# Performance work log

Hardware: AMD Instinct MI355X
Metric: run time of the kernel (lower is better)

Reference implementation:

```python
import jax, jax.numpy as jnp
import numpy as np

N_HEAD = 16

def rel_shift(x):
    # x: (qlen, klen, B, n). Pad one zero column at front of klen axis,
    # reinterpret as (klen+1, qlen, B, n), drop first row, reshape back.
    qlen, klen, b, n = x.shape
    x_pad = jnp.pad(x, ((0, 0), (1, 0), (0, 0), (0, 0)))
    x_pad = x_pad.reshape(klen + 1, qlen, b, n)
    return x_pad[1:].reshape(qlen, klen, b, n)

def setup_inputs() -> dict:
    key = jax.random.key(0)
    ks = jax.random.split(key, 9)
    qlen = klen = 1024
    B = 4
    d_model = 1024
    d_head = d_model // N_HEAD
    q = jax.random.normal(ks[0], (qlen, B, d_model), jnp.float32)
    K = jax.random.normal(ks[1], (klen, B, d_model), jnp.float32)
    V = jax.random.normal(ks[2], (klen, B, d_model), jnp.float32)
    mask = jax.random.bernoulli(ks[3], 0.1, (1, klen, B, 1))
    r = jax.random.normal(ks[4], (klen, d_model), jnp.float32)
    u = jax.random.normal(ks[5], (N_HEAD, d_head), jnp.float32) * 0.02
    v = jax.random.normal(ks[6], (N_HEAD, d_head), jnp.float32) * 0.02
    Wr = jax.random.normal(ks[7], (d_model, d_model), jnp.float32) / np.sqrt(d_model)
    br = jax.random.normal(ks[8], (d_model,), jnp.float32) * 0.02
    return {"q": q, "K": K, "V": V, "mask": mask, "r": r, "u": u, "v": v, "Wr": Wr, "br": br}

def reference(q, K, V, mask, r, u, v, Wr, br):
    qlen, bsz, d_model = q.shape
    klen = K.shape[0]
    d_head = d_model // N_HEAD
    qh = q.reshape(qlen, bsz, N_HEAD, d_head)
    Kh = K.reshape(klen, bsz, N_HEAD, d_head)
    Vh = V.reshape(klen, bsz, N_HEAD, d_head)
    rh = (r @ Wr.T + br).reshape(klen, N_HEAD, d_head)  # r_net projection
    AC = jnp.einsum('ibnd,jbnd->ijbn', qh + u, Kh)
    BD = rel_shift(jnp.einsum('ibnd,jnd->ijbn', qh + v, rh))
    score = (AC + BD) / jnp.sqrt(jnp.asarray(d_head, q.dtype))
    # mask (1,klen,B,1) broadcasts over qlen and heads (torch repeats over heads)
    score = jnp.where(mask, jnp.asarray(-1e9, score.dtype), score)
    weight = jax.nn.softmax(score, axis=1)
    out = jnp.einsum('ijbn,jbnd->ibnd', weight, Vh).reshape(qlen, bsz, d_model)
    return out, weight.mean(axis=-1)
```

## Files before the change

kernel.cpp:

```cpp
#include <hip/hip_runtime.h>
#include <hip/hip_fp16.h>
#include <stdint.h>


#define L 1024
#define BATCH 4
#define NH 16
#define DH 64
#define DM 1024
#define TI 16
#define NJT 16
#define BDP_ST 1032
#define SCALE 0.125f
#define CS 0.18033688011112042f

typedef __attribute__((ext_vector_type(8))) short short8;
typedef __attribute__((ext_vector_type(4))) float f32x4;

static __device__ __forceinline__ unsigned short f2bf(float f) {
    union { float f; unsigned int u; } x; x.f = f;
    return (unsigned short)((x.u + 0x7fffu + ((x.u >> 16) & 1u)) >> 16);
}
static __device__ __forceinline__ float bf2f(unsigned short h) {
    union { unsigned int u; float f; } x; x.u = ((unsigned int)h) << 16;
    return x.f;
}
static __device__ __forceinline__ unsigned short f2h(float f) {
    __half h = __float2half(f);
    union { __half h; unsigned short s; } x; x.h = h; return x.s;
}
static __device__ __forceinline__ float h2f(unsigned short s) {
    union { __half h; unsigned short s; } x; x.s = s; return __half2float(x.h);
}
static __device__ __forceinline__ unsigned short* usp(void* base, int byteoff) {
    return (unsigned short*)((char*)base + byteoff);
}
static __device__ __forceinline__ short8 ld8(const void* base, int byteoff) {
    return *(const short8*)((const char*)base + byteoff);
}
static __device__ __forceinline__ float fexp2(float x) {
#if __has_builtin(__builtin_amdgcn_exp2f)
    return __builtin_amdgcn_exp2f(x);
#else
    return __expf(x * 0.6931471805599453f);
#endif
}
#define SW128(row, colByte) ((((row) * 128) + (colByte)) ^ (((row) & 7) << 4))

__global__ __launch_bounds__(256) void rh_gemm_mfma(
    const float* __restrict__ r, const float* __restrict__ Wr,
    const float* __restrict__ br, unsigned short* __restrict__ rhb)
{
    __shared__ unsigned short rT[64 * 64];
    __shared__ unsigned short wT[64 * 64];
    const int c0 = blockIdx.x * 64, m0 = blockIdx.y * 64;
    const int tid = threadIdx.x;
    const int w = tid >> 6, lane = tid & 63, lr = lane & 15, lg = lane >> 4;
    f32x4 acc[4] = {};

    for (int kt = 0; kt < 16; ++kt) {
        const int k0 = kt * 64;
        __syncthreads();
        const int row = tid >> 2, cb = (tid & 3) * 16;
#pragma unroll
        for (int q4 = 0; q4 < 4; ++q4) {
            float4 rv = *(const float4*)(r + (size_t)(c0 + row) * DM + k0 + cb + q4 * 4);
            unsigned short* p = usp(rT, SW128(row, (cb + q4 * 4) * 2));
            p[0] = f2bf(rv.x); p[1] = f2bf(rv.y); p[2] = f2bf(rv.z); p[3] = f2bf(rv.w);
            float4 wv = *(const float4*)(Wr + (size_t)(m0 + row) * DM + k0 + cb + q4 * 4);
            unsigned short* pw = usp(wT, SW128(row, (cb + q4 * 4) * 2));
            pw[0] = f2bf(wv.x); pw[1] = f2bf(wv.y); pw[2] = f2bf(wv.z); pw[3] = f2bf(wv.w);
        }
        __syncthreads();
#pragma unroll
        for (int mch = 0; mch < 4; ++mch)
#pragma unroll
            for (int kh = 0; kh < 2; ++kh) {
                short8 a  = ld8(rT, SW128(w * 16 + lr,   (kh * 32 + lg * 8) * 2));
                short8 bb = ld8(wT, SW128(mch * 16 + lr, (kh * 32 + lg * 8) * 2));
                acc[mch] = __builtin_amdgcn_mfma_f32_16x16x32_bf16(a, bb, acc[mch], 0, 0, 0);
            }
    }
#pragma unroll
    for (int mch = 0; mch < 4; ++mch)
#pragma unroll
        for (int r2 = 0; r2 < 4; ++r2) {
            const int c = c0 + w * 16 + lg * 4 + r2;
            const int d = mch * 16 + lr;
            const float val = acc[mch][r2] + br[m0 + d];
            rhb[((size_t)blockIdx.y * L + c) * DH + d] = f2bf(val);
        }
}

__global__ __launch_bounds__(256) void rh_gemm_kernel(
    const float* __restrict__ r, const float* __restrict__ Wr,
    const float* __restrict__ br, float* __restrict__ rhf)
{
    __shared__ float As[16][65];
    __shared__ float Bs[16][65];
    const int j0 = blockIdx.x * 64;
    const int m0 = blockIdx.y * 64;
    const int tid = threadIdx.x;
    const int ty = tid >> 4, tx = tid & 15;
    float acc[4][4] = {};

    for (int k0 = 0; k0 < DM; k0 += 16) {
        const int row = tid >> 2, c4 = (tid & 3) << 2;
        float4 av = *(const float4*)(r  + (size_t)(j0 + row) * DM + k0 + c4);
        float4 bv = *(const float4*)(Wr + (size_t)(m0 + row) * DM + k0 + c4);
        __syncthreads();
        As[c4 + 0][row] = av.x; As[c4 + 1][row] = av.y;
        As[c4 + 2][row] = av.z; As[c4 + 3][row] = av.w;
        Bs[c4 + 0][row] = bv.x; Bs[c4 + 1][row] = bv.y;
        Bs[c4 + 2][row] = bv.z; Bs[c4 + 3][row] = bv.w;
        __syncthreads();
#pragma unroll
        for (int k = 0; k < 16; ++k) {
            float a[4], bb[4];
#pragma unroll
            for (int t = 0; t < 4; ++t) { a[t] = As[k][ty * 4 + t]; bb[t] = Bs[k][tx * 4 + t]; }
#pragma unroll
            for (int ii = 0; ii < 4; ++ii)
#pragma unroll
                for (int jj = 0; jj < 4; ++jj)
                    acc[ii][jj] = fmaf(a[ii], bb[jj], acc[ii][jj]);
        }
    }
#pragma unroll
    for (int ii = 0; ii < 4; ++ii) {
        const int row = j0 + ty * 4 + ii;
#pragma unroll
        for (int jj = 0; jj < 4; ++jj) {
            const int col = m0 + tx * 4 + jj;
            rhf[(size_t)row * DM + col] = acc[ii][jj] + br[col];
        }
    }
}

__global__ __launch_bounds__(256) void prepass_kernel(
    const float* __restrict__ Kg, const float* __restrict__ Vg,
    unsigned short* __restrict__ Kbf, unsigned short* __restrict__ Vtb)
{
    __shared__ unsigned short tile[64][80];
    const int j0 = blockIdx.x * 64;
    const int b = blockIdx.y, n = blockIdx.z;
    const int bn = b * NH + n;
    const int tid = threadIdx.x;

    for (int idx = tid; idx < 64 * 16; idx += 256) {
        const int jr = idx >> 4, s4 = (idx & 15) * 4;
        const size_t src = ((size_t)(j0 + jr) * BATCH + b) * DM + n * DH + s4;
        float4 kv = *(const float4*)(Kg + src);
        ushort4 o;
        o.x = f2bf(kv.x); o.y = f2bf(kv.y); o.z = f2bf(kv.z); o.w = f2bf(kv.w);
        *(ushort4*)(Kbf + ((size_t)bn * L + j0 + jr) * DH + s4) = o;
        float4 vv4 = *(const float4*)(Vg + src);
        tile[s4 + 0][jr] = f2bf(vv4.x); tile[s4 + 1][jr] = f2bf(vv4.y);
        tile[s4 + 2][jr] = f2bf(vv4.z); tile[s4 + 3][jr] = f2bf(vv4.w);
    }
    __syncthreads();
    for (int idx = tid; idx < 64 * 8; idx += 256) {
        const int d = idx >> 3, p8 = (idx & 7) * 8;
        short8 o = *(const short8*)&tile[d][p8];
        *(short8*)(Vtb + ((size_t)bn * DH + d) * L + j0 + p8) = o;
    }
}

__global__ __launch_bounds__(256) void wm_reduce_kernel(
    const unsigned short* __restrict__ Wf, const float* __restrict__ rdeng,
    float* __restrict__ wm_out)
{
    const int ig = blockIdx.x;
    const int b  = blockIdx.y;
    const int ib = ig >> 2, lg = ig & 3;
    const int tid = threadIdx.x;
#pragma unroll
    for (int jj = 0; jj < 4; ++jj) {
        const int j = jj * 256 + tid;
        const int gc = j >> 4, lr = j & 15;
        float a0 = 0.f, a1 = 0.f, a2 = 0.f, a3 = 0.f;
#pragma unroll
        for (int n = 0; n < NH; ++n) {
            const int bn = b * NH + n;
            const float4 rd = *(const float4*)(rdeng + ((size_t)bn << 10) + ig * 4);
            ushort4 wv = *(const ushort4*)(Wf +
                ((((size_t)bn * 64 + ib) * 64 + gc) * 64 + lg * 16 + lr) * 4);
            a0 += bf2f(wv.x) * rd.x; a1 += bf2f(wv.y) * rd.y;
            a2 += bf2f(wv.z) * rd.z; a3 += bf2f(wv.w) * rd.w;
        }
        const size_t o = ((size_t)(ig * 4) * L + j) * BATCH + b;
        wm_out[o]                      = a0;
        wm_out[o + (size_t)L * BATCH]  = a1;
        wm_out[o + 2 * (size_t)L * BATCH] = a2;
        wm_out[o + 3 * (size_t)L * BATCH] = a3;
    }
}

__global__ __launch_bounds__(256, 3) void attn_fused(
    const float* __restrict__ q,
    const unsigned short* __restrict__ Kbf, const unsigned short* __restrict__ Vtb,
    const unsigned char* __restrict__ maskp,
    const float* __restrict__ uu, const float* __restrict__ vvp,
    const unsigned short* __restrict__ rhb,
    float* __restrict__ out, unsigned short* __restrict__ W_ws,
    float* __restrict__ rdeng)
{
    __shared__ __align__(16) unsigned short BDp[17 * BDP_ST];
    __shared__ __align__(16) unsigned short Wt[4][2][16 * 64];
    __shared__ unsigned char mblk[L];
    __shared__ float denomP[4][16];
    __shared__ float rdenom[16];
    __shared__ int mflags;

    const int lin = blockIdx.x;
    const int xcd = lin & 7, idx = lin >> 3;
    const int ib  = idx & 63;
    const int pane = xcd * 8 + (idx >> 6);
    const int b = pane >> 4, n = pane & 15;
    const int i0 = ib * 16;
    const int bn = pane;

    const int tid = threadIdx.x;
    const int w = tid >> 6, lane = tid & 63, lr = lane & 15, lg = lane >> 4;

    if (tid == 0) mflags = 0;
    __syncthreads();
    {
        int local = 0;
        for (int ww = tid; ww < 1024; ww += 256) {
            const unsigned int word = ((const unsigned int*)maskp)[ww];
            if (word == 0x3f800000u) local |= 1;
            else if (word & 0xffffff00u) local |= 2;
        }
        if (local) atomicOr(&mflags, local);
    }
    __syncthreads();
    {
        const int mtype = (mflags & 1) ? 2 : ((mflags & 2) ? 1 : 0);
        for (int j = tid; j < L; j += 256) {
            bool mv;
            if (mtype == 2)      mv = ((const float*)maskp)[j * BATCH + b] != 0.f;
            else if (mtype == 1) mv = maskp[j * BATCH + b] != 0;
            else                 mv = ((const int*)maskp)[j * BATCH + b] != 0;
            mblk[j] = mv ? 1 : 0;
        }
    }
    if (tid < 17 * 8) {
        const int row = tid >> 3, cp = tid & 7;
        BDp[row * BDP_ST + 1024 + cp] = 0;
    }

    const float* qrow = q + ((size_t)(i0 + lr) * BATCH + b) * DM + n * DH;
    const float* urow = uu + n * DH;
    const float* vrow = vvp + n * DH;
    short8 qu_a[2], qv_a[2];
#pragma unroll
    for (int kh = 0; kh < 2; ++kh) {
        const int kb = kh * 32 + lg * 8;
        float4 qa = *(const float4*)(qrow + kb), qb = *(const float4*)(qrow + kb + 4);
        float4 ua = *(const float4*)(urow + kb), ub = *(const float4*)(urow + kb + 4);
        float4 va = *(const float4*)(vrow + kb), vb = *(const float4*)(vrow + kb + 4);
        short8 su, sv;
        su[0] = (short)f2bf((qa.x + ua.x) * CS); su[1] = (short)f2bf((qa.y + ua.y) * CS);
        su[2] = (short)f2bf((qa.z + ua.z) * CS); su[3] = (short)f2bf((qa.w + ua.w) * CS);
        su[4] = (short)f2bf((qb.x + ub.x) * CS); su[5] = (short)f2bf((qb.y + ub.y) * CS);
        su[6] = (short)f2bf((qb.z + ub.z) * CS); su[7] = (short)f2bf((qb.w + ub.w) * CS);
        sv[0] = (short)f2bf((qa.x + va.x) * CS); sv[1] = (short)f2bf((qa.y + va.y) * CS);
        sv[2] = (short)f2bf((qa.z + va.z) * CS); sv[3] = (short)f2bf((qa.w + va.w) * CS);
        sv[4] = (short)f2bf((qb.x + vb.x) * CS); sv[5] = (short)f2bf((qb.y + vb.y) * CS);
        sv[6] = (short)f2bf((qb.z + vb.z) * CS); sv[7] = (short)f2bf((qb.w + vb.w) * CS);
        qu_a[kh] = su; qv_a[kh] = sv;
    }
    float qv16[16];
    {
        const int kq = (tid & 3) * 16;
        if (i0 + 16 < L) {
            const float* q16 = q + ((size_t)(i0 + 16) * BATCH + b) * DM + n * DH;
#pragma unroll
            for (int e4 = 0; e4 < 4; ++e4) {
                float4 qa = *(const float4*)(q16 + kq + e4 * 4);
                float4 va = *(const float4*)(vrow + kq + e4 * 4);
                qv16[e4 * 4 + 0] = (qa.x + va.x) * CS; qv16[e4 * 4 + 1] = (qa.y + va.y) * CS;
                qv16[e4 * 4 + 2] = (qa.z + va.z) * CS; qv16[e4 * 4 + 3] = (qa.w + va.w) * CS;
            }
        } else {
#pragma unroll
            for (int e = 0; e < 16; ++e) qv16[e] = 0.f;
        }
    }

    {
        const unsigned short* rpane = rhb + (size_t)n * L * DH;
        const int ccol = w * 16 + lr;
        short8 rb[2][2];
#pragma unroll
        for (int kh = 0; kh < 2; ++kh) {
            rb[0][kh] = *(const short8*)(rpane + (size_t)ccol * DH + kh * 32 + lg * 8);
            rb[1][kh] = *(const short8*)(rpane + (size_t)(64 + ccol) * DH + kh * 32 + lg * 8);
        }
        const int col16 = tid >> 2;
        const int kq = (tid & 3) * 16;
#pragma unroll
        for (int ct = 0; ct < 16; ++ct) {
            const int c0 = ct * 64;
            const int cur = ct & 1;
            short8 nk0, nk1;
            if (ct + 2 < 16) {
                nk0 = *(const short8*)(rpane + (size_t)((ct + 2) * 64 + ccol) * DH + lg * 8);
                nk1 = *(const short8*)(rpane + (size_t)((ct + 2) * 64 + ccol) * DH + 32 + lg * 8);
            }
            f32x4 acc = {0.f, 0.f, 0.f, 0.f};
#pragma unroll
            for (int kh = 0; kh < 2; ++kh)
                acc = __builtin_amdgcn_mfma_f32_16x16x32_bf16(qv_a[kh], rb[cur][kh], acc, 0, 0, 0);
#pragma unroll
            for (int r2 = 0; r2 < 4; ++r2)
                BDp[(lg * 4 + r2) * BDP_ST + c0 + ccol] = f2h(acc[r2]);
            {
                short8 ra0 = *(const short8*)(rpane + (size_t)(c0 + col16) * DH + kq);
                short8 ra1 = *(const short8*)(rpane + (size_t)(c0 + col16) * DH + kq + 8);
                float s16 = 0.f;
#pragma unroll
                for (int e = 0; e < 8; ++e) {
                    s16 = fmaf(qv16[e],     bf2f((unsigned short)ra0[e]), s16);
                    s16 = fmaf(qv16[e + 8], bf2f((unsigned short)ra1[e]), s16);
                }
                s16 += __shfl_xor(s16, 1);
                s16 += __shfl_xor(s16, 2);
                if ((tid & 3) == 0) BDp[16 * BDP_ST + c0 + col16] = f2h(s16);
            }
            if (ct + 2 < 16) { rb[cur][0] = nk0; rb[cur][1] = nk1; }
        }
    }
    __syncthreads();

    const unsigned short* Kpane = Kbf + (size_t)bn * L * DH;
    const unsigned short* Vpane = Vtb + (size_t)bn * DH * L;
    const int jwbase = w * 256;
    f32x4 pv[4] = {};
    float dl[4] = {0.f, 0.f, 0.f, 0.f};
    int ilb[4];
#pragma unroll
    for (int r2 = 0; r2 < 4; ++r2) ilb[r2] = (lg * 4 + r2) * BDP_ST;

    short8 kf[2][2];
#pragma unroll
    for (int kh = 0; kh < 2; ++kh) {
        kf[0][kh] = *(const short8*)(Kpane + (size_t)(jwbase + lr) * DH + kh * 32 + lg * 8);
        kf[1][kh] = *(const short8*)(Kpane + (size_t)(jwbase + 16 + lr) * DH + kh * 32 + lg * 8);
    }

#pragma unroll 1
    for (int sub = 0; sub < 4; ++sub) {
        const int jbase = jwbase + sub * 64;
        unsigned short* WtW = &Wt[w][sub & 1][0];
        short8 vfr[8];
#pragma unroll
        for (int dch = 0; dch < 4; ++dch)
#pragma unroll
            for (int kh = 0; kh < 2; ++kh)
                vfr[dch * 2 + kh] = *(const short8*)(Vpane + (size_t)(dch * 16 + lr) * L + jbase + kh * 32 + lg * 8);
#pragma unroll
        for (int c4 = 0; c4 < 4; ++c4) {
            const int chunk = sub * 4 + c4;
            const int cur = c4 & 1;
            short8 nk0, nk1;
            if (chunk + 2 < 16) {
                const int jn = jwbase + (chunk + 2) * 16 + lr;
                nk0 = *(const short8*)(Kpane + (size_t)jn * DH + lg * 8);
                nk1 = *(const short8*)(Kpane + (size_t)jn * DH + 32 + lg * 8);
            }
            f32x4 acc = {0.f, 0.f, 0.f, 0.f};
#pragma unroll
            for (int kh = 0; kh < 2; ++kh)
                acc = __builtin_amdgcn_mfma_f32_16x16x32_bf16(qu_a[kh], kf[cur][kh], acc, 0, 0, 0);
            const int gj = jbase + c4 * 16 + lr;
            const float mo = mblk[gj] ? -1e9f : 0.f;
            const int ebase = gj - i0 - lg * 4;
            ushort4 wpack;
#pragma unroll
            for (int r2 = 0; r2 < 4; ++r2) {
                const int e = ebase - r2;
                const int addr = ilb[r2] + e + ((e <= 0) ? 1023 : 1030);
                const float bd = h2f(BDp[addr]);
                float s = fminf(acc[r2] + bd + mo, 126.f);
                const float wg = fexp2(s);
                dl[r2] += wg;
                const unsigned short wb = f2bf(wg);
                ((unsigned short*)&wpack)[r2] = wb;
                *usp(WtW, SW128(lg * 4 + r2, (c4 * 16 + lr) * 2)) = wb;
            }
            {
                const int gc = w * 16 + chunk - w * 16 + jwbase / 16 + 0;
                const int gcc = (jbase >> 4) + c4;
                *(ushort4*)(W_ws + ((((size_t)bn * 64 + ib) * 64 + gcc) * 64 + lane) * 4) = wpack;
                (void)gc;
            }
            if (chunk + 2 < 16) { kf[cur][0] = nk0; kf[cur][1] = nk1; }
        }
#pragma unroll
        for (int dch = 0; dch < 4; ++dch)
#pragma unroll
            for (int kh = 0; kh < 2; ++kh) {
                short8 a = ld8(WtW, SW128(lr, (kh * 32 + lg * 8) * 2));
                pv[dch] = __builtin_amdgcn_mfma_f32_16x16x32_bf16(a, vfr[dch * 2 + kh], pv[dch], 0, 0, 0);
            }
    }

#pragma unroll
    for (int r2 = 0; r2 < 4; ++r2) {
        float d = dl[r2];
        d += __shfl_xor(d, 1); d += __shfl_xor(d, 2);
        d += __shfl_xor(d, 4); d += __shfl_xor(d, 8);
        if (lr == 0) denomP[w][lg * 4 + r2] = d;
    }
    {
        float* pvw = (float*)&Wt[w][0][0];
#pragma unroll
        for (int dch = 0; dch < 4; ++dch)
#pragma unroll
            for (int r2 = 0; r2 < 4; ++r2)
                pvw[(lg * 4 + r2) * 64 + dch * 16 + lr] = pv[dch][r2];
    }
    __syncthreads();
    if (tid < 16) {
        const float dn = denomP[0][tid] + denomP[1][tid] + denomP[2][tid] + denomP[3][tid];
        rdenom[tid] = 1.f / dn;
        rdeng[((size_t)bn << 10) + i0 + tid] = 1.f / (dn * 16.f);
    }
    __syncthreads();

    {
        const float* pvwAll = (const float*)&Wt[0][0][0];
        const int il = tid >> 4, d0 = (tid & 15) * 4;
        float4 o  = *(const float4*)(pvwAll + 0 * 1024 + il * 64 + d0);
        float4 o1 = *(const float4*)(pvwAll + 1 * 1024 + il * 64 + d0);
        float4 o2 = *(const float4*)(pvwAll + 2 * 1024 + il * 64 + d0);
        float4 o3 = *(const float4*)(pvwAll + 3 * 1024 + il * 64 + d0);
        const float rs = rdenom[il];
        o.x = (o.x + o1.x + o2.x + o3.x) * rs;
        o.y = (o.y + o1.y + o2.y + o3.y) * rs;
        o.z = (o.z + o1.z + o2.z + o3.z) * rs;
        o.w = (o.w + o1.w + o2.w + o3.w) * rs;
        *(float4*)(out + ((size_t)(i0 + il) * BATCH + b) * DM + n * DH + d0) = o;
    }
}

template<int MODE>
__global__ __launch_bounds__(256, 2) void attn_legacy(
    const float* __restrict__ q,
    const void* __restrict__ Kp, const void* __restrict__ Vp,
    const unsigned char* __restrict__ maskp,
    const float* __restrict__ uu, const float* __restrict__ vvp,
    const void* __restrict__ rhp,
    float* __restrict__ out, float* __restrict__ wm_out)
{
    __shared__ unsigned short QU[16 * 64];
    __shared__ unsigned short QV[17 * 64];
    __shared__ unsigned short KR[(MODE == 1) ? 64 * 64 : 8];
    __shared__ unsigned short VT[(MODE == 1) ? 64 * 64 : 8];
    __shared__ unsigned short BDp[17 * BDP_ST];
    __shared__ unsigned short Wt[2][16 * 64];
    __shared__ unsigned char mblk[L];
    __shared__ float denomP[4][16];
    __shared__ float rdenom[16];
    __shared__ int mflags;

    const int i0 = blockIdx.x * TI;
    const int b  = blockIdx.y;
    const int n  = blockIdx.z;
    const int bn = b * NH + n;
    const int tid = threadIdx.x;
    const int w = tid >> 6, lane = tid & 63, lr = lane & 15, lg = lane >> 4;

    const unsigned short* Kbf = (const unsigned short*)Kp;
    const unsigned short* Vtb = (const unsigned short*)Vp;
    const unsigned short* rhb = (const unsigned short*)rhp;
    const float* Kg  = (const float*)Kp;
    const float* Vg  = (const float*)Vp;
    const float* rhf = (const float*)rhp;

    if (tid == 0) mflags = 0;
    __syncthreads();
    {
        int local = 0;
        for (int ww = tid; ww < 1024; ww += 256) {
            const unsigned int word = ((const unsigned int*)maskp)[ww];
            if (word == 0x3f800000u) local |= 1;
            else if (word & 0xffffff00u) local |= 2;
        }
        if (local) atomicOr(&mflags, local);
    }
    __syncthreads();
    {
        const int mtype = (mflags & 1) ? 2 : ((mflags & 2) ? 1 : 0);
        for (int j = tid; j < L; j += 256) {
            bool mv;
            if (mtype == 2)      mv = ((const float*)maskp)[j * BATCH + b] != 0.f;
            else if (mtype == 1) mv = maskp[j * BATCH + b] != 0;
            else                 mv = ((const int*)maskp)[j * BATCH + b] != 0;
            mblk[j] = mv ? 1 : 0;
        }
    }
    for (int idx = tid; idx < 17 * 64; idx += 256) {
        const int row = idx >> 6, d = idx & 63;
        const int gi = i0 + row;
        const float qval = (gi < L) ? q[((size_t)gi * BATCH + b) * DM + n * DH + d] : 0.f;
        *usp(QV, SW128(row, d * 2)) = f2bf((qval + vvp[n * DH + d]) * SCALE);
        if (row < 16) *usp(QU, SW128(row, d * 2)) = f2bf((qval + uu[n * DH + d]) * SCALE);
    }
    __syncthreads();

    for (int ct = 0; ct < 16; ++ct) {
        const int c0 = ct * 64;
        const int ccol = w * 16 + lr;
        if constexpr (MODE == 1) {
            __syncthreads();
            for (int idx = tid; idx < 64 * 16; idx += 256) {
                const int cr = idx >> 4, d4 = (idx & 15) * 4;
                float4 rv = *(const float4*)(rhf + (size_t)(c0 + cr) * DM + n * DH + d4);
                unsigned short* p = usp(KR, SW128(cr, d4 * 2));
                p[0] = f2bf(rv.x); p[1] = f2bf(rv.y); p[2] = f2bf(rv.z); p[3] = f2bf(rv.w);
            }
            __syncthreads();
        }
        f32x4 acc = {0.f, 0.f, 0.f, 0.f};
#pragma unroll
        for (int kh = 0; kh < 2; ++kh) {
            short8 a = ld8(QV, SW128(lr, (kh * 32 + lg * 8) * 2));
            short8 bb;
            if constexpr (MODE == 0)
                bb = *(const short8*)(rhb + ((size_t)n * L + c0 + ccol) * DH + kh * 32 + lg * 8);
            else
                bb = ld8(KR, SW128(ccol, (kh * 32 + lg * 8) * 2));
            acc = __builtin_amdgcn_mfma_f32_16x16x32_bf16(a, bb, acc, 0, 0, 0);
        }
#pragma unroll
        for (int r2 = 0; r2 < 4; ++r2)
            BDp[(lg * 4 + r2) * BDP_ST + c0 + ccol] = f2h(acc[r2]);
        {
            const int col = tid >> 2, kq = (tid & 3) * 16;
            float s16 = 0.f;
#pragma unroll
            for (int kk = 0; kk < 16; kk += 8) {
                short8 qa = ld8(QV, SW128(16, (kq + kk) * 2));
                short8 ra;
                if constexpr (MODE == 0)
                    ra = *(const short8*)(rhb + ((size_t)n * L + c0 + col) * DH + kq + kk);
                else
                    ra = ld8(KR, SW128(col, (kq + kk) * 2));
#pragma unroll
                for (int e = 0; e < 8; ++e)
                    s16 = fmaf(bf2f((unsigned short)qa[e]), bf2f((unsigned short)ra[e]), s16);
            }
            s16 += __shfl_xor(s16, 1);
            s16 += __shfl_xor(s16, 2);
            if ((tid & 3) == 0) BDp[16 * BDP_ST + c0 + col] = f2h(s16);
        }
    }

    const int jloc = w * 16 + lr;
    __syncthreads();

    f32x4 pv = {0.f, 0.f, 0.f, 0.f};
    float dl[4] = {0.f, 0.f, 0.f, 0.f};
    float tmp[4][NJT];
#pragma unroll
    for (int jt = 0; jt < NJT; ++jt) {
        const int j0 = jt * 64;
        const int gj = j0 + jloc;
        const int cur = jt & 1;
        if constexpr (MODE == 1) {
            __syncthreads();
            for (int idx = tid; idx < 64 * 16; idx += 256) {
                const int jr = idx >> 4, d4 = (idx & 15) * 4;
                const size_t src = ((size_t)(j0 + jr) * BATCH + b) * DM + n * DH + d4;
                float4 kv = *(const float4*)(Kg + src);
                unsigned short* p = usp(KR, SW128(jr, d4 * 2));
                p[0] = f2bf(kv.x); p[1] = f2bf(kv.y); p[2] = f2bf(kv.z); p[3] = f2bf(kv.w);
                float4 vv4 = *(const float4*)(Vg + src);
                *usp(VT, SW128(d4 + 0, jr * 2)) = f2bf(vv4.x);
                *usp(VT, SW128(d4 + 1, jr * 2)) = f2bf(vv4.y);
                *usp(VT, SW128(d4 + 2, jr * 2)) = f2bf(vv4.z);
                *usp(VT, SW128(d4 + 3, jr * 2)) = f2bf(vv4.w);
            }
            __syncthreads();
        }
        f32x4 acc = {0.f, 0.f, 0.f, 0.f};
#pragma unroll
        for (int kh = 0; kh < 2; ++kh) {
            short8 a = ld8(QU, SW128(lr, (kh * 32 + lg * 8) * 2));
            short8 bb;
            if constexpr (MODE == 0)
                bb = *(const short8*)(Kbf + ((size_t)bn * L + gj) * DH + kh * 32 + lg * 8);
            else
                bb = ld8(KR, SW128(jloc, (kh * 32 + lg * 8) * 2));
            acc = __builtin_amdgcn_mfma_f32_16x16x32_bf16(a, bb, acc, 0, 0, 0);
        }
        const bool msk = mblk[gj] != 0;
#pragma unroll
        for (int r2 = 0; r2 < 4; ++r2) {
            const int il = lg * 4 + r2;
            const int gi = i0 + il;
            const int t = gj - gi;
            float bd = 0.f;
            if (t != 1) {
                const int c = (t <= 0) ? (L - 1 + t) : (t - 2);
                bd = h2f(BDp[(il + (t >= 1 ? 1 : 0)) * BDP_ST + c]);
            }
            float s = acc[r2] + bd;
            if (msk) s = -1e9f;
            const float wgt = __expf(fminf(s, 80.f));
            dl[r2] += wgt;
            tmp[r2][jt] = wgt;
            *usp(Wt[cur], SW128(il, jloc * 2)) = f2bf(wgt);
        }
        __syncthreads();
#pragma unroll
        for (int kh = 0; kh < 2; ++kh) {
            short8 a = ld8(Wt[cur], SW128(lr, (kh * 32 + lg * 8) * 2));
            short8 bb;
            if constexpr (MODE == 0)
                bb = *(const short8*)(Vtb + ((size_t)bn * DH + jloc) * L + j0 + kh * 32 + lg * 8);
            else
                bb = ld8(VT, SW128(jloc, (kh * 32 + lg * 8) * 2));
            pv = __builtin_amdgcn_mfma_f32_16x16x32_bf16(a, bb, pv, 0, 0, 0);
        }
    }

#pragma unroll
    for (int r2 = 0; r2 < 4; ++r2) {
        float d = dl[r2];
        d += __shfl_xor(d, 1); d += __shfl_xor(d, 2);
        d += __shfl_xor(d, 4); d += __shfl_xor(d, 8);
        if (lr == 0) denomP[w][lg * 4 + r2] = d;
    }
    __syncthreads();
    if (tid < 16)
        rdenom[tid] = 1.f / (denomP[0][tid] + denomP[1][tid] + denomP[2][tid] + denomP[3][tid]);
    __syncthreads();

#pragma unroll
    for (int r2 = 0; r2 < 4; ++r2) {
        const int il = lg * 4 + r2;
        out[((size_t)(i0 + il) * BATCH + b) * DM + n * DH + w * 16 + lr] = pv[r2] * rdenom[il];
    }
#pragma unroll
    for (int r2 = 0; r2 < 4; ++r2) {
        const int il = lg * 4 + r2;
        const float rs = rdenom[il] * (1.f / 16.f);
#pragma unroll
        for (int jt = 0; jt < NJT; ++jt)
            atomicAdd(wm_out + ((size_t)(i0 + il) * L + jt * 64 + jloc) * BATCH + b,
                      tmp[r2][jt] * rs);
    }
}

extern "C" void kernel_launch(void* const* d_in, const int* in_sizes, int n_in,
                              void* d_out, int out_size, void* d_ws, size_t ws_size,
                              hipStream_t stream)
{
    (void)in_sizes; (void)n_in; (void)out_size;
    const float* q   = (const float*)d_in[0];
    const float* K   = (const float*)d_in[1];
    const float* V   = (const float*)d_in[2];
    const unsigned char* mask = (const unsigned char*)d_in[3];
    const float* r   = (const float*)d_in[4];
    const float* u   = (const float*)d_in[5];
    const float* v   = (const float*)d_in[6];
    const float* Wr  = (const float*)d_in[7];
    const float* br  = (const float*)d_in[8];

    float* out = (float*)d_out;
    float* wm  = out + (size_t)L * BATCH * DM;

    const size_t kvbytes = (size_t)BATCH * NH * L * DH * 2;
    const size_t rhbytes = (size_t)NH * L * DH * 2;
    const size_t wmbytes = (size_t)BATCH * NH * L * L * 2;
    const size_t rdbytes = (size_t)BATCH * NH * L * 4;

    if (ws_size >= 2 * kvbytes + rhbytes + wmbytes + rdbytes) {
        unsigned short* Kbf = (unsigned short*)d_ws;
        unsigned short* Vtb = Kbf + kvbytes / 2;
        unsigned short* rhb = Vtb + kvbytes / 2;
        unsigned short* Wws = rhb + rhbytes / 2;
        float* rdeng = (float*)(Wws + wmbytes / 2);
        rh_gemm_mfma<<<dim3(16, 16), 256, 0, stream>>>(r, Wr, br, rhb);
        prepass_kernel<<<dim3(16, 4, 16), 256, 0, stream>>>(K, V, Kbf, Vtb);
        attn_fused<<<dim3(4096), 256, 0, stream>>>(
            q, Kbf, Vtb, mask, u, v, rhb, out, Wws, rdeng);
        wm_reduce_kernel<<<dim3(256, BATCH), 256, 0, stream>>>(Wws, rdeng, wm);
    } else if (ws_size >= 2 * kvbytes + rhbytes) {
        hipMemsetAsync(wm, 0, (size_t)L * L * BATCH * sizeof(float), stream);
        unsigned short* Kbf = (unsigned short*)d_ws;
        unsigned short* Vtb = Kbf + kvbytes / 2;
        unsigned short* rhb = Vtb + kvbytes / 2;
        rh_gemm_mfma<<<dim3(16, 16), 256, 0, stream>>>(r, Wr, br, rhb);
        prepass_kernel<<<dim3(16, 4, 16), 256, 0, stream>>>(K, V, Kbf, Vtb);
        attn_legacy<0><<<dim3(64, 4, 16), 256, 0, stream>>>(
            q, Kbf, Vtb, mask, u, v, rhb, out, wm);
    } else {
        hipMemsetAsync(wm, 0, (size_t)L * L * BATCH * sizeof(float), stream);
        float* rhf = (float*)d_ws;
        rh_gemm_kernel<<<dim3(16, 16), 256, 0, stream>>>(r, Wr, br, rhf);
        attn_legacy<1><<<dim3(64, 4, 16), 256, 0, stream>>>(
            q, K, V, mask, u, v, rhf, out, wm);
    }
}
```

Before: 287.0 us.

## Pre-shift BD into final layout, transpose QK MFMA, shrink LDS for occupancy

The BD (positional) scores are now written straight into rel-shifted positions in a 16x1024 LDS buffer, so the softmax loop reads four contiguous values per lane instead of doing per-element shifted address math. The QK MFMA swaps its operands so each lane holds consecutive key columns, which allows vectorized mask and BD reads and a single per-lane denominator accumulator. The W tile is processed in 32-column windows with a smaller LDS buffer, and the PV scratch reuses the BD buffer; the lower LDS use lets launch bounds rise to 4 blocks per CU. The wm_reduce kernel is remapped to one block per query row so its output stores are contiguous, at the cost of four times as many blocks.

Measured after the change: 421.8 us. 1.47x slower.

```diff
diff --git a/kernel.cpp b/kernel.cpp
--- a/kernel.cpp
+++ b/kernel.cpp
@@ -10,7 +10,9 @@
 #define DM 1024
 #define TI 16
 #define NJT 16
+#define BD_ST 1028
 #define BDP_ST 1032
+#define WT_ST 40
 #define SCALE 0.125f
 #define CS 0.18033688011112042f
 
@@ -170,33 +172,30 @@
     const unsigned short* __restrict__ Wf, const float* __restrict__ rdeng,
     float* __restrict__ wm_out)
 {
-    const int ig = blockIdx.x;
-    const int b  = blockIdx.y;
-    const int ib = ig >> 2, lg = ig & 3;
-    const int tid = threadIdx.x;
-#pragma unroll
-    for (int jj = 0; jj < 4; ++jj) {
-        const int j = jj * 256 + tid;
-        const int gc = j >> 4, lr = j & 15;
-        float a0 = 0.f, a1 = 0.f, a2 = 0.f, a3 = 0.f;
-#pragma unroll
-        for (int n = 0; n < NH; ++n) {
-            const int bn = b * NH + n;
-            const float4 rd = *(const float4*)(rdeng + ((size_t)bn << 10) + ig * 4);
-            ushort4 wv = *(const ushort4*)(Wf +
-                ((((size_t)bn * 64 + ib) * 64 + gc) * 64 + lg * 16 + lr) * 4);
-            a0 += bf2f(wv.x) * rd.x; a1 += bf2f(wv.y) * rd.y;
-            a2 += bf2f(wv.z) * rd.z; a3 += bf2f(wv.w) * rd.w;
-        }
-        const size_t o = ((size_t)(ig * 4) * L + j) * BATCH + b;
-        wm_out[o]                      = a0;
-        wm_out[o + (size_t)L * BATCH]  = a1;
-        wm_out[o + 2 * (size_t)L * BATCH] = a2;
-        wm_out[o + 3 * (size_t)L * BATCH] = a3;
-    }
-}
-
-__global__ __launch_bounds__(256, 3) void attn_fused(
+    const int i = blockIdx.x;
+    const int b = blockIdx.y;
+    const int ib = i >> 4, lr = i & 15;
+    const int j0 = threadIdx.x * 4;
+    const int gc = j0 >> 4, lg = (j0 >> 2) & 3;
+    const int lane = lg * 16 + lr;
+    float a0 = 0.f, a1 = 0.f, a2 = 0.f, a3 = 0.f;
+#pragma unroll
+    for (int n = 0; n < NH; ++n) {
+        const int bn = b * NH + n;
+        const float rd = rdeng[((size_t)bn << 10) + i];
+        ushort4 wv = *(const ushort4*)(Wf +
+            ((((size_t)bn * 64 + ib) * 64 + gc) * 64 + lane) * 4);
+        a0 += bf2f(wv.x) * rd; a1 += bf2f(wv.y) * rd;
+        a2 += bf2f(wv.z) * rd; a3 += bf2f(wv.w) * rd;
+    }
+    const size_t o = ((size_t)i * L + j0) * BATCH + b;
+    wm_out[o]             = a0;
+    wm_out[o + BATCH]     = a1;
+    wm_out[o + 2 * BATCH] = a2;
+    wm_out[o + 3 * BATCH] = a3;
+}
+
+__global__ __launch_bounds__(256, 4) void attn_fused(
     const float* __restrict__ q,
     const unsigned short* __restrict__ Kbf, const unsigned short* __restrict__ Vtb,
     const unsigned char* __restrict__ maskp,
@@ -205,8 +204,8 @@
     float* __restrict__ out, unsigned short* __restrict__ W_ws,
     float* __restrict__ rdeng)
 {
-    __shared__ __align__(16) unsigned short BDp[17 * BDP_ST];
-    __shared__ __align__(16) unsigned short Wt[4][2][16 * 64];
+    __shared__ __align__(16) unsigned short BD[16 * BD_ST];
+    __shared__ __align__(16) unsigned short Wt[4][16 * WT_ST];
     __shared__ unsigned char mblk[L];
     __shared__ float denomP[4][16];
     __shared__ float rdenom[16];
@@ -245,9 +244,9 @@
             mblk[j] = mv ? 1 : 0;
         }
     }
-    if (tid < 17 * 8) {
-        const int row = tid >> 3, cp = tid & 7;
-        BDp[row * BDP_ST + 1024 + cp] = 0;
+    if (tid < 16) {
+        const int jz = i0 + tid + 1;
+        if (jz <= 1023) BD[tid * BD_ST + jz] = 0;
     }
 
     const float* qrow = q + ((size_t)(i0 + lr) * BATCH + b) * DM + n * DH;
@@ -313,9 +312,16 @@
 #pragma unroll
             for (int kh = 0; kh < 2; ++kh)
                 acc = __builtin_amdgcn_mfma_f32_16x16x32_bf16(qv_a[kh], rb[cur][kh], acc, 0, 0, 0);
-#pragma unroll
-            for (int r2 = 0; r2 < 4; ++r2)
-                BDp[(lg * 4 + r2) * BDP_ST + c0 + ccol] = f2h(acc[r2]);
+            const int c = c0 + ccol;
+#pragma unroll
+            for (int r2 = 0; r2 < 4; ++r2) {
+                const int ilp = lg * 4 + r2;
+                const unsigned short hv = f2h(acc[r2]);
+                const int j1 = c + i0 + ilp - 1023;
+                if (j1 >= 0) BD[ilp * BD_ST + j1] = hv;
+                const int j2 = c + i0 + ilp + 1;
+                if (ilp >= 1 && j2 <= 1023) BD[(ilp - 1) * BD_ST + j2] = hv;
+            }
             {
                 short8 ra0 = *(const short8*)(rpane + (size_t)(c0 + col16) * DH + kq);
                 short8 ra1 = *(const short8*)(rpane + (size_t)(c0 + col16) * DH + kq + 8);
@@ -327,7 +333,9 @@
                 }
                 s16 += __shfl_xor(s16, 1);
                 s16 += __shfl_xor(s16, 2);
-                if ((tid & 3) == 0) BDp[16 * BDP_ST + c0 + col16] = f2h(s16);
+                const int j16 = c0 + col16 + i0 + 17;
+                if ((tid & 3) == 0 && j16 <= 1023)
+                    BD[15 * BD_ST + j16] = f2h(s16);
             }
             if (ct + 2 < 16) { rb[cur][0] = nk0; rb[cur][1] = nk1; }
         }
@@ -337,11 +345,10 @@
     const unsigned short* Kpane = Kbf + (size_t)bn * L * DH;
     const unsigned short* Vpane = Vtb + (size_t)bn * DH * L;
     const int jwbase = w * 256;
+    unsigned short* WtW = &Wt[w][0];
     f32x4 pv[4] = {};
-    float dl[4] = {0.f, 0.f, 0.f, 0.f};
-    int ilb[4];
-#pragma unroll
-    for (int r2 = 0; r2 < 4; ++r2) ilb[r2] = (lg * 4 + r2) * BDP_ST;
+    float dl = 0.f;
+    const size_t wsbase = (((size_t)bn * 64 + ib) * 64) * 64 * 4;
 
     short8 kf[2][2];
 #pragma unroll
@@ -353,76 +360,66 @@
 #pragma unroll 1
     for (int sub = 0; sub < 4; ++sub) {
         const int jbase = jwbase + sub * 64;
-        unsigned short* WtW = &Wt[w][sub & 1][0];
-        short8 vfr[8];
-#pragma unroll
-        for (int dch = 0; dch < 4; ++dch)
-#pragma unroll
-            for (int kh = 0; kh < 2; ++kh)
-                vfr[dch * 2 + kh] = *(const short8*)(Vpane + (size_t)(dch * 16 + lr) * L + jbase + kh * 32 + lg * 8);
-#pragma unroll
-        for (int c4 = 0; c4 < 4; ++c4) {
-            const int chunk = sub * 4 + c4;
-            const int cur = c4 & 1;
-            short8 nk0, nk1;
-            if (chunk + 2 < 16) {
-                const int jn = jwbase + (chunk + 2) * 16 + lr;
-                nk0 = *(const short8*)(Kpane + (size_t)jn * DH + lg * 8);
-                nk1 = *(const short8*)(Kpane + (size_t)jn * DH + 32 + lg * 8);
-            }
-            f32x4 acc = {0.f, 0.f, 0.f, 0.f};
-#pragma unroll
-            for (int kh = 0; kh < 2; ++kh)
-                acc = __builtin_amdgcn_mfma_f32_16x16x32_bf16(qu_a[kh], kf[cur][kh], acc, 0, 0, 0);
-            const int gj = jbase + c4 * 16 + lr;
-            const float mo = mblk[gj] ? -1e9f : 0.f;
-            const int ebase = gj - i0 - lg * 4;
-            ushort4 wpack;
-#pragma unroll
-            for (int r2 = 0; r2 < 4; ++r2) {
-                const int e = ebase - r2;
-                const int addr = ilb[r2] + e + ((e <= 0) ? 1023 : 1030);
-                const float bd = h2f(BDp[addr]);
-                float s = fminf(acc[r2] + bd + mo, 126.f);
-                const float wg = fexp2(s);
-                dl[r2] += wg;
-                const unsigned short wb = f2bf(wg);
-                ((unsigned short*)&wpack)[r2] = wb;
-                *usp(WtW, SW128(lg * 4 + r2, (c4 * 16 + lr) * 2)) = wb;
-            }
-            {
-                const int gc = w * 16 + chunk - w * 16 + jwbase / 16 + 0;
-                const int gcc = (jbase >> 4) + c4;
-                *(ushort4*)(W_ws + ((((size_t)bn * 64 + ib) * 64 + gcc) * 64 + lane) * 4) = wpack;
-                (void)gc;
-            }
-            if (chunk + 2 < 16) { kf[cur][0] = nk0; kf[cur][1] = nk1; }
-        }
-#pragma unroll
-        for (int dch = 0; dch < 4; ++dch)
-#pragma unroll
-            for (int kh = 0; kh < 2; ++kh) {
-                short8 a = ld8(WtW, SW128(lr, (kh * 32 + lg * 8) * 2));
-                pv[dch] = __builtin_amdgcn_mfma_f32_16x16x32_bf16(a, vfr[dch * 2 + kh], pv[dch], 0, 0, 0);
-            }
-    }
-
-#pragma unroll
-    for (int r2 = 0; r2 < 4; ++r2) {
-        float d = dl[r2];
-        d += __shfl_xor(d, 1); d += __shfl_xor(d, 2);
-        d += __shfl_xor(d, 4); d += __shfl_xor(d, 8);
-        if (lr == 0) denomP[w][lg * 4 + r2] = d;
-    }
+#pragma unroll
+        for (int win = 0; win < 2; ++win) {
+            short8 vf[4];
+#pragma unroll
+            for (int dch = 0; dch < 4; ++dch)
+                vf[dch] = *(const short8*)(Vpane + (size_t)(dch * 16 + lr) * L
+                                           + jbase + win * 32 + lg * 8);
+#pragma unroll
+            for (int cc = 0; cc < 2; ++cc) {
+                const int chunk = sub * 4 + win * 2 + cc;
+                const int cur = chunk & 1;
+                short8 nk0, nk1;
+                if (chunk + 2 < 16) {
+                    const int jn = jwbase + (chunk + 2) * 16 + lr;
+                    nk0 = *(const short8*)(Kpane + (size_t)jn * DH + lg * 8);
+                    nk1 = *(const short8*)(Kpane + (size_t)jn * DH + 32 + lg * 8);
+                }
+                f32x4 acc = {0.f, 0.f, 0.f, 0.f};
+#pragma unroll
+                for (int kh = 0; kh < 2; ++kh)
+                    acc = __builtin_amdgcn_mfma_f32_16x16x32_bf16(kf[cur][kh], qu_a[kh], acc, 0, 0, 0);
+                const int jc = jbase + win * 32 + cc * 16;
+                const int jq = jc + lg * 4;
+                const unsigned int m4 = *(const unsigned int*)&mblk[jq];
+                const ushort4 bdq = *(const ushort4*)&BD[lr * BD_ST + jq];
+                ushort4 wpack;
+#pragma unroll
+                for (int r2 = 0; r2 < 4; ++r2) {
+                    const unsigned short bdh =
+                        (r2 == 0) ? bdq.x : (r2 == 1) ? bdq.y : (r2 == 2) ? bdq.z : bdq.w;
+                    const float mo = ((m4 >> (8 * r2)) & 0xffu) ? -1e9f : 0.f;
+                    const float s = fminf(acc[r2] + h2f(bdh) + mo, 126.f);
+                    const float wg = fexp2(s);
+                    dl += wg;
+                    ((unsigned short*)&wpack)[r2] = f2bf(wg);
+                }
+                *(ushort4*)(WtW + lr * WT_ST + cc * 16 + lg * 4) = wpack;
+                *(ushort4*)(W_ws + wsbase + (((size_t)(jc >> 4)) * 64 + lane) * 4) = wpack;
+                if (chunk + 2 < 16) { kf[cur][0] = nk0; kf[cur][1] = nk1; }
+            }
+            short8 afrag = *(const short8*)(WtW + lr * WT_ST + lg * 8);
+#pragma unroll
+            for (int dch = 0; dch < 4; ++dch)
+                pv[dch] = __builtin_amdgcn_mfma_f32_16x16x32_bf16(afrag, vf[dch], pv[dch], 0, 0, 0);
+        }
+    }
+
+    dl += __shfl_xor(dl, 16, 64);
+    dl += __shfl_xor(dl, 32, 64);
+    if (lane < 16) denomP[w][lane] = dl;
+    __syncthreads();
+
     {
-        float* pvw = (float*)&Wt[w][0][0];
+        float* pvw = (float*)BD + w * 1024;
 #pragma unroll
         for (int dch = 0; dch < 4; ++dch)
 #pragma unroll
             for (int r2 = 0; r2 < 4; ++r2)
                 pvw[(lg * 4 + r2) * 64 + dch * 16 + lr] = pv[dch][r2];
     }
-    __syncthreads();
     if (tid < 16) {
         const float dn = denomP[0][tid] + denomP[1][tid] + denomP[2][tid] + denomP[3][tid];
         rdenom[tid] = 1.f / dn;
@@ -431,7 +428,7 @@
     __syncthreads();
 
     {
-        const float* pvwAll = (const float*)&Wt[0][0][0];
+        const float* pvwAll = (const float*)BD;
         const int il = tid >> 4, d0 = (tid & 15) * 4;
         float4 o  = *(const float4*)(pvwAll + 0 * 1024 + il * 64 + d0);
         float4 o1 = *(const float4*)(pvwAll + 1 * 1024 + il * 64 + d0);
@@ -689,7 +686,7 @@
         prepass_kernel<<<dim3(16, 4, 16), 256, 0, stream>>>(K, V, Kbf, Vtb);
         attn_fused<<<dim3(4096), 256, 0, stream>>>(
             q, Kbf, Vtb, mask, u, v, rhb, out, Wws, rdeng);
-        wm_reduce_kernel<<<dim3(256, BATCH), 256, 0, stream>>>(Wws, rdeng, wm);
+        wm_reduce_kernel<<<dim3(L, BATCH), 256, 0, stream>>>(Wws, rdeng, wm);
     } else if (ws_size >= 2 * kvbytes + rhbytes) {
         hipMemsetAsync(wm, 0, (size_t)L * L * BATCH * sizeof(float), stream);
         unsigned short* Kbf = (unsigned short*)d_ws;
```
